# Kernel optimization log

Measured on AMD Instinct MI355X. Metric: run time of the kernel, lower is better.

The kernel has to match this reference:

```python
import jax, jax.numpy as jnp
import numpy as np

IMG_W, IMG_H = 128, 128
N_PTS = 256
MIN_D, MAX_D = 2.0, 6.0
FOCAL = 1.7320508  # 1/tan(fov/2), fov=60deg (FoVPerspectiveCameras default)
SCALING = 0.1      # scaling_factor default
EPS_EA = 1e-10     # pytorch3d EmissionAbsorptionRaymarcher eps


def setup_inputs() -> dict:
    key = jax.random.key(0)
    k1, k2 = jax.random.split(key)
    image3d = jax.random.uniform(k1, (1, 1, 128, 128, 128), jnp.float32)
    opacity = jax.random.uniform(k2, (1, 1, 128, 128, 128), jnp.float32)
    # row-vector camera convention (pytorch3d): p_cam = p_world @ R + T
    R = jnp.zeros((1, 3, 3), jnp.float32).at[:, jnp.arange(3), jnp.arange(3)].set(1.0)
    T = jnp.zeros((1, 3), jnp.float32).at[:, 2].set(4.0)
    return {"image3d": image3d, "opacity": opacity, "R": R, "T": T}


def _trilinear(vol, pts):
    """vol [C,D,H,W]; pts [N,3] xyz in [-1,1] (x->W, y->H, z->D).
    align_corners=True, zero padding outside. Returns [N,C]."""
    C, D, H, W = vol.shape
    x = (pts[:, 0] + 1.0) * 0.5 * (W - 1)
    y = (pts[:, 1] + 1.0) * 0.5 * (H - 1)
    z = (pts[:, 2] + 1.0) * 0.5 * (D - 1)
    x0 = jnp.floor(x); y0 = jnp.floor(y); z0 = jnp.floor(z)
    wx = x - x0; wy = y - y0; wz = z - z0
    vol_flat = vol.reshape(C, -1)
    out = jnp.zeros((pts.shape[0], C), vol.dtype)
    for dz in (0, 1):
        for dy in (0, 1):
            for dx in (0, 1):
                xi = (x0 + dx).astype(jnp.int32)
                yi = (y0 + dy).astype(jnp.int32)
                zi = (z0 + dz).astype(jnp.int32)
                valid = ((xi >= 0) & (xi < W) & (yi >= 0) & (yi < H)
                         & (zi >= 0) & (zi < D))
                w = ((wx if dx else 1.0 - wx) * (wy if dy else 1.0 - wy)
                     * (wz if dz else 1.0 - wz)) * valid.astype(vol.dtype)
                idx = ((jnp.clip(zi, 0, D - 1) * H + jnp.clip(yi, 0, H - 1)) * W
                       + jnp.clip(xi, 0, W - 1))
                vals = jnp.take(vol_flat, idx, axis=1)  # [C,N]
                out = out + w[:, None] * vals.T
    return out


def _forward(image3d, opacity, R, T):
    B = image3d.shape[0]
    features_vol = jnp.repeat(image3d, 3, axis=1)            # [B,3,D,H,W]
    densities_vol = opacity * SCALING                        # [B,1,D,H,W]
    Dv, Hv, Wv = image3d.shape[2:]
    shape = max(image3d.shape[1], image3d.shape[2])
    voxel = 3.0 / shape
    half_extent = voxel * (jnp.array([Wv, Hv, Dv], jnp.float32) - 1.0) / 2.0

    # NDC pixel grid (pytorch3d: +x left, +y up)
    xs = jnp.linspace(1.0, -1.0, IMG_W)
    ys = jnp.linspace(1.0, -1.0, IMG_H)
    gy, gx = jnp.meshgrid(ys, xs, indexing="ij")             # [H,W]
    dirs_cam = jnp.stack([gx / FOCAL, gy / FOCAL, jnp.ones_like(gx)], -1)  # [H,W,3]
    depths = jnp.linspace(MIN_D, MAX_D, N_PTS)               # [P]

    # row-vector transforms: p_world = (p_cam - T) @ R^T
    origins = jnp.einsum("bi,bji->bj", -T, R)                # camera centers [B,3]
    dirs_world = jnp.einsum("hwi,bji->bhwj", dirs_cam, R)    # [B,H,W,3]
    pts = (origins[:, None, None, None, :]
           + depths[None, None, None, :, None] * dirs_world[:, :, :, None, :])
    local = pts / half_extent                                # [B,H,W,P,3]

    pts_flat = local.reshape(B, -1, 3)
    feats = jax.vmap(_trilinear)(features_vol, pts_flat)
    feats = feats.reshape(B, IMG_H, IMG_W, N_PTS, 3)
    dens = jax.vmap(_trilinear)(densities_vol, pts_flat)
    dens = dens.reshape(B, IMG_H, IMG_W, N_PTS)

    # EmissionAbsorption raymarcher
    cum = jnp.cumprod((1.0 + EPS_EA) - dens, axis=-1)
    absorption = jnp.concatenate([jnp.ones_like(cum[..., :1]), cum[..., :-1]], -1)
    weights = dens * absorption
    feat_out = jnp.sum(weights[..., None] * feats, axis=-2)  # [B,H,W,3]
    opac = 1.0 - jnp.prod(1.0 - dens, axis=-1, keepdims=True)
    rgba = jnp.concatenate([feat_out, opac], axis=-1)        # [B,H,W,4]

    screen = jnp.transpose(rgba, (0, 3, 2, 1))               # permute(0,3,2,1)
    gray = screen[:, :3].mean(axis=1, keepdims=True)         # [B,1,W,H]
    st = (gray - gray.mean()) / (gray.std(ddof=1) + 1e-8)    # standardized
    out = (st - st.min() + 1e-8) / (st.max() - st.min() + 1e-8)  # normalized
    return out


def reference(image3d, opacity, R, T):
    return _forward(image3d, opacity, R, T)
```

## Files before the change

### kernel.cpp

```cpp
#include <hip/hip_runtime.h>
#include <math.h>


#define FOCAL 1.7320508f

typedef struct __attribute__((packed, aligned(4))) { float a, b; } f2u;

__global__ __launch_bounds__(1024) void dvr_kernel(
    const float* __restrict__ img, const float* __restrict__ opa,
    const float* __restrict__ Rm, const float* __restrict__ Tv,
    float* __restrict__ g, double* __restrict__ bstats,
    unsigned int* __restrict__ counter, float* __restrict__ out)
{
  const int tid  = threadIdx.x;
  const int lane = tid & 63;
  const int seg  = tid >> 6;
  const int B    = blockIdx.x;
  const int b    = ((B & 7) << 5) | (B >> 3);
  const int h    = b >> 1;
  const int w    = ((b & 1) << 6) | lane;

  const float R00=Rm[0], R01=Rm[1], R02=Rm[2];
  const float R10=Rm[3], R11=Rm[4], R12=Rm[5];
  const float R20=Rm[6], R21=Rm[7], R22=Rm[8];
  const float T0=Tv[0], T1=Tv[1], T2=Tv[2];

  const float ox = -(T0*R00 + T1*R01 + T2*R02);
  const float oy = -(T0*R10 + T1*R11 + T2*R12);
  const float oz = -(T0*R20 + T1*R21 + T2*R22);

  const float gx = 1.0f - (2.0f/127.0f) * (float)w;
  const float gy = 1.0f - (2.0f/127.0f) * (float)h;
  const float dcx = gx * (1.0f/FOCAL);
  const float dcy = gy * (1.0f/FOCAL);
  const float dwx = dcx*R00 + dcy*R01 + R02;
  const float dwy = dcx*R10 + dcy*R11 + R12;
  const float dwz = dcx*R20 + dcy*R21 + R22;

  const float s_he = (1.0f/1.48828125f) * 63.5f;
  const float ax = dwx * s_he, bxc = ox * s_he + 63.5f;
  const float ay = dwy * s_he, byc = oy * s_he + 63.5f;
  const float az = dwz * s_he, bzc = oz * s_he + 63.5f;

  const int p0 = seg << 4;

  float lp = 1.0f;
  float accl = 0.0f;

  #pragma unroll 4
  for (int j = 0; j < 16; ++j) {
    const float depth = 2.0f + (4.0f/255.0f) * (float)(p0 + j);
    const float x = bxc + depth * ax;
    const float y = byc + depth * ay;
    const float z = bzc + depth * az;
    const float x0f = floorf(x), y0f = floorf(y), z0f = floorf(z);
    const float wx = x - x0f, wy = y - y0f, wz = z - z0f;
    const int x0 = (int)x0f, y0 = (int)y0f, z0 = (int)z0f;

    float feat = 0.0f, dens = 0.0f;
    if (x0 >= -1 && x0 <= 127 && y0 >= -1 && y0 <= 127 &&
        z0 >= -1 && z0 <= 127) {
      const float fx0 = (x0 >= 0)   ? (1.0f - wx) : 0.0f;
      const float fx1 = (x0 <= 126) ? wx          : 0.0f;
      const float fy0 = (y0 >= 0)   ? (1.0f - wy) : 0.0f;
      const float fy1 = (y0 <= 126) ? wy          : 0.0f;
      const float fz0 = (z0 >= 0)   ? (1.0f - wz) : 0.0f;
      const float fz1 = (z0 <= 126) ? wz          : 0.0f;
      const int iy0 = ((y0 >= 0)   ? y0     : 0)   << 7;
      const int iy1 = ((y0 <= 126) ? y0 + 1 : 127) << 7;
      const int iz0 = ((z0 >= 0)   ? z0     : 0)   << 14;
      const int iz1 = ((z0 <= 126) ? z0 + 1 : 127) << 14;
      const int ixp = (x0 >= 0) ? ((x0 <= 126) ? x0 : 126) : 0;

      const int b00 = iz0 + iy0 + ixp, b01 = iz0 + iy1 + ixp;
      const int b10 = iz1 + iy0 + ixp, b11 = iz1 + iy1 + ixp;
      const float w00 = fz0*fy0, w01 = fz0*fy1, w10 = fz1*fy0, w11 = fz1*fy1;

      const f2u q00 = *(const f2u*)(img + b00);
      const f2u q01 = *(const f2u*)(img + b01);
      const f2u q10 = *(const f2u*)(img + b10);
      const f2u q11 = *(const f2u*)(img + b11);
      const f2u r00 = *(const f2u*)(opa + b00);
      const f2u r01 = *(const f2u*)(opa + b01);
      const f2u r10 = *(const f2u*)(opa + b10);
      const f2u r11 = *(const f2u*)(opa + b11);

      const bool cA = (x0 < 127);
      const bool cB = (x0 >= 0);

      feat = w00*(fx0*(cA ? q00.a : q00.b) + fx1*(cB ? q00.b : q00.a))
           + w01*(fx0*(cA ? q01.a : q01.b) + fx1*(cB ? q01.b : q01.a))
           + w10*(fx0*(cA ? q10.a : q10.b) + fx1*(cB ? q10.b : q10.a))
           + w11*(fx0*(cA ? q11.a : q11.b) + fx1*(cB ? q11.b : q11.a));
      dens = w00*(fx0*(cA ? r00.a : r00.b) + fx1*(cB ? r00.b : r00.a))
           + w01*(fx0*(cA ? r01.a : r01.b) + fx1*(cB ? r01.b : r01.a))
           + w10*(fx0*(cA ? r10.a : r10.b) + fx1*(cB ? r10.b : r10.a))
           + w11*(fx0*(cA ? r11.a : r11.b) + fx1*(cB ? r11.b : r11.a));
    }
    const float d = dens * 0.1f;
    accl += feat * d * lp;
    lp   *= (1.0f - d);
  }

  __shared__ float2 slp[16][64];
  slp[seg][lane] = make_float2(accl, lp);
  __syncthreads();

  if (tid < 64) {
    float T = 1.0f, acc = 0.0f;
    #pragma unroll
    for (int s = 0; s < 16; ++s) {
      const float2 v = slp[s][tid];
      acc += v.x * T;
      T *= v.y;
    }
    const int ww = ((b & 1) << 6) | tid;
    g[(ww << 7) + h] = acc;

    double sum = (double)acc;
    double sq  = (double)acc * (double)acc;
    float mn = acc, mx = acc;
    #pragma unroll
    for (int off = 32; off >= 1; off >>= 1) {
      sum += __shfl_xor(sum, off, 64);
      sq  += __shfl_xor(sq,  off, 64);
      mn = fminf(mn, __shfl_xor(mn, off, 64));
      mx = fmaxf(mx, __shfl_xor(mx, off, 64));
    }
    if (tid == 0) {
      bstats[(b << 2) + 0] = sum;
      bstats[(b << 2) + 1] = sq;
      bstats[(b << 2) + 2] = (double)mn;
      bstats[(b << 2) + 3] = (double)mx;
    }
  }
  __syncthreads();

  __shared__ int is_last;
  if (tid == 0) {
    __threadfence();
    const unsigned int old = atomicAdd(counter, 1u);
    const unsigned int base = old - 255u;
    is_last = (base == 0xAAAAAAAAu || base == 0u) ? 1 : 0;
  }
  __syncthreads();
  if (!is_last) return;
  __threadfence();

  double S = 0.0, Q = 0.0;
  float MN = 3.402823466e38f, MX = -3.402823466e38f;
  if (tid < 256) {
    S  = bstats[(tid << 2) + 0];
    Q  = bstats[(tid << 2) + 1];
    MN = (float)bstats[(tid << 2) + 2];
    MX = (float)bstats[(tid << 2) + 3];
  }
  #pragma unroll
  for (int off = 32; off >= 1; off >>= 1) {
    S += __shfl_xor(S, off, 64);
    Q += __shfl_xor(Q, off, 64);
    MN = fminf(MN, __shfl_xor(MN, off, 64));
    MX = fmaxf(MX, __shfl_xor(MX, off, 64));
  }
  __shared__ double rs[16], rq[16];
  __shared__ float rmn[16], rmx[16];
  if (lane == 0) { rs[seg] = S; rq[seg] = Q; rmn[seg] = MN; rmx[seg] = MX; }
  __syncthreads();

  __shared__ float cs[3];
  if (tid == 0) {
    double St = 0.0, Qt = 0.0;
    float MNt = rmn[0], MXt = rmx[0];
    #pragma unroll
    for (int i = 0; i < 4; ++i) {
      St += rs[i]; Qt += rq[i];
      MNt = fminf(MNt, rmn[i]); MXt = fmaxf(MXt, rmx[i]);
    }
    const double mean = St / 16384.0;
    double var = (Qt - 16384.0 * mean * mean) / 16383.0;
    if (var < 0.0) var = 0.0;
    const float sdev = (float)sqrt(var) + 1e-8f;
    cs[0] = MNt;
    cs[1] = 1.0f / sdev;
    cs[2] = 1.0f / ((MXt - MNt) / sdev + 1e-8f);
  }
  __syncthreads();

  const float mnv = cs[0], invs = cs[1], sc = cs[2];
  for (int i = tid; i < 16384; i += 1024) {
    out[i] = ((g[i] - mnv) * invs + 1e-8f) * sc;
  }
}

extern "C" void kernel_launch(void* const* d_in, const int* in_sizes, int n_in,
                              void* d_out, int out_size, void* d_ws, size_t ws_size,
                              hipStream_t stream) {
  const float* img = (const float*)d_in[0];
  const float* opa = (const float*)d_in[1];
  const float* Rm  = (const float*)d_in[2];
  const float* Tv  = (const float*)d_in[3];
  float* out = (float*)d_out;

  char* wsb = (char*)d_ws;
  float*        g       = (float*)wsb;
  double*       bstats  = (double*)(wsb + 65536);
  unsigned int* counter = (unsigned int*)(wsb + 65536 + 8192);

  dvr_kernel<<<256, 1024, 0, stream>>>(img, opa, Rm, Tv, g, bstats, counter, out);
}
```

Before: 94.33 us.

## Pack image and opacity into interleaved fp16 volume before raymarching

```diff
diff --git a/kernel.cpp b/kernel.cpp
--- a/kernel.cpp
+++ b/kernel.cpp
@@ -1,13 +1,38 @@
 #include <hip/hip_runtime.h>
+#include <hip/hip_fp16.h>
 #include <math.h>
 
 
 #define FOCAL 1.7320508f
 
-typedef struct __attribute__((packed, aligned(4))) { float a, b; } f2u;
+typedef struct __attribute__((packed, aligned(4))) { unsigned int lo, hi; } u2u;
+
+static __device__ __forceinline__ float2 h2f(unsigned int u) {
+  __half2 h = *reinterpret_cast<__half2*>(&u);
+  return __half22float2(h);
+}
+
+__global__ __launch_bounds__(256) void pack_kernel(
+    const float4* __restrict__ img, const float4* __restrict__ opa,
+    uint4* __restrict__ dst)
+{
+  const int i = blockIdx.x * 256 + threadIdx.x;
+  const float4 f = img[i];
+  const float4 o = opa[i];
+  const __half2 h0 = __floats2half2_rn(f.x, o.x);
+  const __half2 h1 = __floats2half2_rn(f.y, o.y);
+  const __half2 h2 = __floats2half2_rn(f.z, o.z);
+  const __half2 h3 = __floats2half2_rn(f.w, o.w);
+  uint4 r;
+  r.x = *(const unsigned int*)&h0;
+  r.y = *(const unsigned int*)&h1;
+  r.z = *(const unsigned int*)&h2;
+  r.w = *(const unsigned int*)&h3;
+  dst[i] = r;
+}
 
 __global__ __launch_bounds__(1024) void dvr_kernel(
-    const float* __restrict__ img, const float* __restrict__ opa,
+    const unsigned int* __restrict__ vol,
     const float* __restrict__ Rm, const float* __restrict__ Tv,
     float* __restrict__ g, double* __restrict__ bstats,
     unsigned int* __restrict__ counter, float* __restrict__ out)
@@ -76,26 +101,32 @@
       const int b10 = iz1 + iy0 + ixp, b11 = iz1 + iy1 + ixp;
       const float w00 = fz0*fy0, w01 = fz0*fy1, w10 = fz1*fy0, w11 = fz1*fy1;
 
-      const f2u q00 = *(const f2u*)(img + b00);
-      const f2u q01 = *(const f2u*)(img + b01);
-      const f2u q10 = *(const f2u*)(img + b10);
-      const f2u q11 = *(const f2u*)(img + b11);
-      const f2u r00 = *(const f2u*)(opa + b00);
-      const f2u r01 = *(const f2u*)(opa + b01);
-      const f2u r10 = *(const f2u*)(opa + b10);
-      const f2u r11 = *(const f2u*)(opa + b11);
+      const u2u q00 = *(const u2u*)(vol + b00);
+      const u2u q01 = *(const u2u*)(vol + b01);
+      const u2u q10 = *(const u2u*)(vol + b10);
+      const u2u q11 = *(const u2u*)(vol + b11);
 
       const bool cA = (x0 < 127);
       const bool cB = (x0 >= 0);
 
-      feat = w00*(fx0*(cA ? q00.a : q00.b) + fx1*(cB ? q00.b : q00.a))
-           + w01*(fx0*(cA ? q01.a : q01.b) + fx1*(cB ? q01.b : q01.a))
-           + w10*(fx0*(cA ? q10.a : q10.b) + fx1*(cB ? q10.b : q10.a))
-           + w11*(fx0*(cA ? q11.a : q11.b) + fx1*(cB ? q11.b : q11.a));
-      dens = w00*(fx0*(cA ? r00.a : r00.b) + fx1*(cB ? r00.b : r00.a))
-           + w01*(fx0*(cA ? r01.a : r01.b) + fx1*(cB ? r01.b : r01.a))
-           + w10*(fx0*(cA ? r10.a : r10.b) + fx1*(cB ? r10.b : r10.a))
-           + w11*(fx0*(cA ? r11.a : r11.b) + fx1*(cB ? r11.b : r11.a));
+      const unsigned int a00 = cA ? q00.lo : q00.hi, b00s = cB ? q00.hi : q00.lo;
+      const unsigned int a01 = cA ? q01.lo : q01.hi, b01s = cB ? q01.hi : q01.lo;
+      const unsigned int a10 = cA ? q10.lo : q10.hi, b10s = cB ? q10.hi : q10.lo;
+      const unsigned int a11 = cA ? q11.lo : q11.hi, b11s = cB ? q11.hi : q11.lo;
+
+      const float2 fa00 = h2f(a00), fb00 = h2f(b00s);
+      const float2 fa01 = h2f(a01), fb01 = h2f(b01s);
+      const float2 fa10 = h2f(a10), fb10 = h2f(b10s);
+      const float2 fa11 = h2f(a11), fb11 = h2f(b11s);
+
+      feat = w00*(fx0*fa00.x + fx1*fb00.x)
+           + w01*(fx0*fa01.x + fx1*fb01.x)
+           + w10*(fx0*fa10.x + fx1*fb10.x)
+           + w11*(fx0*fa11.x + fx1*fb11.x);
+      dens = w00*(fx0*fa00.y + fx1*fb00.y)
+           + w01*(fx0*fa01.y + fx1*fb01.y)
+           + w10*(fx0*fa10.y + fx1*fb10.y)
+           + w11*(fx0*fa11.y + fx1*fb11.y);
     }
     const float d = dens * 0.1f;
     accl += feat * d * lp;
@@ -205,6 +236,9 @@
   float*        g       = (float*)wsb;
   double*       bstats  = (double*)(wsb + 65536);
   unsigned int* counter = (unsigned int*)(wsb + 65536 + 8192);
-
-  dvr_kernel<<<256, 1024, 0, stream>>>(img, opa, Rm, Tv, g, bstats, counter, out);
-}
+  unsigned int* vol     = (unsigned int*)(wsb + (1 << 20));
+
+  pack_kernel<<<2048, 256, 0, stream>>>((const float4*)img, (const float4*)opa,
+                                        (uint4*)vol);
+  dvr_kernel<<<256, 1024, 0, stream>>>(vol, Rm, Tv, g, bstats, counter, out);
+}
```

Result: slower. 98.75 us (+4.7%).

## Stage per-chunk volume bricks in shared memory as packed half2

Applied to the files above, without the earlier changes.

```diff
diff --git a/kernel.cpp b/kernel.cpp
--- a/kernel.cpp
+++ b/kernel.cpp
@@ -1,10 +1,19 @@
 #include <hip/hip_runtime.h>
+#include <hip/hip_fp16.h>
 #include <math.h>
 
 
 #define FOCAL 1.7320508f
 
-typedef struct __attribute__((packed, aligned(4))) { float a, b; } f2u;
+#define BZ 12
+#define BYW 4
+#define BW 176
+#define ROWSTRIDE (BYW*BW)
+
+static __device__ __forceinline__ float2 h2f(unsigned int u) {
+  __half2 h = *reinterpret_cast<__half2*>(&u);
+  return __half22float2(h);
+}
 
 __global__ __launch_bounds__(1024) void dvr_kernel(
     const float* __restrict__ img, const float* __restrict__ opa,
@@ -14,7 +23,7 @@
 {
   const int tid  = threadIdx.x;
   const int lane = tid & 63;
-  const int seg  = tid >> 6;
+  const int sub  = tid >> 6;
   const int B    = blockIdx.x;
   const int b    = ((B & 7) << 5) | (B >> 3);
   const int h    = b >> 1;
@@ -42,14 +51,64 @@
   const float ay = dwy * s_he, byc = oy * s_he + 63.5f;
   const float az = dwz * s_he, bzc = oz * s_he + 63.5f;
 
-  const int p0 = seg << 4;
-
-  float lp = 1.0f;
-  float accl = 0.0f;
-
-  #pragma unroll 4
-  for (int j = 0; j < 16; ++j) {
-    const float depth = 2.0f + (4.0f/255.0f) * (float)(p0 + j);
+  __shared__ unsigned int brick[BZ*ROWSTRIDE];
+  __shared__ float2 slp[16][64];
+
+  float rayAcc = 0.0f, rayT = 1.0f;
+
+  const float dstep = 4.0f/255.0f;
+
+  #pragma unroll 1
+  for (int c = 0; c < 16; ++c) {
+    const float dA = 2.0f + dstep * (float)(c << 4);
+    const float dB = 2.0f + dstep * (float)((c << 4) + 15);
+    const float xAe = bxc + dA*ax, xBe = bxc + dB*ax;
+    const float yAe = byc + dA*ay, yBe = byc + dB*ay;
+    const float zAe = bzc + dA*az, zBe = bzc + dB*az;
+
+    float xmn = fminf(xAe, xBe), xmx = fmaxf(xAe, xBe);
+    float ymnA = yAe, ymnB = yBe;
+    float zmn = fminf(zAe, zBe), zmx = fmaxf(zAe, zBe);
+    #pragma unroll
+    for (int off = 32; off >= 1; off >>= 1) {
+      xmn  = fminf(xmn,  __shfl_xor(xmn,  off, 64));
+      xmx  = fmaxf(xmx,  __shfl_xor(xmx,  off, 64));
+      ymnA = fminf(ymnA, __shfl_xor(ymnA, off, 64));
+      ymnB = fminf(ymnB, __shfl_xor(ymnB, off, 64));
+      zmn  = fminf(zmn,  __shfl_xor(zmn,  off, 64));
+      zmx  = fmaxf(zmx,  __shfl_xor(zmx,  off, 64));
+    }
+    const int x_lo = (int)floorf(xmn);
+    const int z_lo = (int)floorf(zmn);
+    int zcnt = (int)floorf(zmx) + 2 - z_lo;
+    zcnt = (zcnt < 1) ? 1 : ((zcnt > BZ) ? BZ : zcnt);
+
+    const float zg = zBe - zAe;
+    const float invzg = (fabsf(zg) > 1e-6f) ? (1.0f / zg) : 0.0f;
+    const float ySlope = (ymnB - ymnA) * invzg;
+
+    const bool live = (zmx >= -1.0f) && (zmn <= 128.0f) &&
+                      (xmx >= -1.0f) && (xmn <= 128.0f);
+
+    if (live) {
+      const int n = zcnt * ROWSTRIDE;
+      for (int idx = tid; idx < n; idx += 1024) {
+        const int dz = idx / ROWSTRIDE;
+        const int r2 = idx - dz * ROWSTRIDE;
+        const int dy = r2 / BW;
+        const int dx = r2 - dy * BW;
+        const int ylos = (int)floorf(ymnA + ((float)(z_lo + dz) + 0.5f - zAe) * ySlope) - 1;
+        int gz_ = z_lo + dz;  gz_ = (gz_ < 0) ? 0 : ((gz_ > 127) ? 127 : gz_);
+        int gy_ = ylos + dy;  gy_ = (gy_ < 0) ? 0 : ((gy_ > 127) ? 127 : gy_);
+        int gx_ = x_lo + dx;  gx_ = (gx_ < 0) ? 0 : ((gx_ > 127) ? 127 : gx_);
+        const int a = (((gz_ << 7) + gy_) << 7) + gx_;
+        const __half2 hp = __floats2half2_rn(img[a], opa[a]);
+        brick[idx] = *(const unsigned int*)&hp;
+      }
+    }
+    __syncthreads();
+
+    const float depth = 2.0f + dstep * (float)((c << 4) + sub);
     const float x = bxc + depth * ax;
     const float y = byc + depth * ay;
     const float z = bzc + depth * az;
@@ -66,54 +125,57 @@
       const float fy1 = (y0 <= 126) ? wy          : 0.0f;
       const float fz0 = (z0 >= 0)   ? (1.0f - wz) : 0.0f;
       const float fz1 = (z0 <= 126) ? wz          : 0.0f;
-      const int iy0 = ((y0 >= 0)   ? y0     : 0)   << 7;
-      const int iy1 = ((y0 <= 126) ? y0 + 1 : 127) << 7;
-      const int iz0 = ((z0 >= 0)   ? z0     : 0)   << 14;
-      const int iz1 = ((z0 <= 126) ? z0 + 1 : 127) << 14;
-      const int ixp = (x0 >= 0) ? ((x0 <= 126) ? x0 : 126) : 0;
-
-      const int b00 = iz0 + iy0 + ixp, b01 = iz0 + iy1 + ixp;
-      const int b10 = iz1 + iy0 + ixp, b11 = iz1 + iy1 + ixp;
+
+      int bx = x0 - x_lo;  bx = (bx < 0) ? 0 : ((bx > BW-2) ? (BW-2) : bx);
+      int bz0 = z0 - z_lo; bz0 = (bz0 < 0) ? 0 : ((bz0 > zcnt-1) ? (zcnt-1) : bz0);
+      int bz1 = bz0 + 1;   bz1 = (bz1 > zcnt-1) ? (zcnt-1) : bz1;
+
+      const int ylo0 = (int)floorf(ymnA + ((float)(z_lo + bz0) + 0.5f - zAe) * ySlope) - 1;
+      const int ylo1 = (int)floorf(ymnA + ((float)(z_lo + bz1) + 0.5f - zAe) * ySlope) - 1;
+      int dy00 = y0     - ylo0; dy00 = (dy00 < 0) ? 0 : ((dy00 > 3) ? 3 : dy00);
+      int dy01 = y0 + 1 - ylo0; dy01 = (dy01 < 0) ? 0 : ((dy01 > 3) ? 3 : dy01);
+      int dy10 = y0     - ylo1; dy10 = (dy10 < 0) ? 0 : ((dy10 > 3) ? 3 : dy10);
+      int dy11 = y0 + 1 - ylo1; dy11 = (dy11 < 0) ? 0 : ((dy11 > 3) ? 3 : dy11);
+
+      const int e00 = (bz0*BYW + dy00)*BW + bx;
+      const int e01 = (bz0*BYW + dy01)*BW + bx;
+      const int e10 = (bz1*BYW + dy10)*BW + bx;
+      const int e11 = (bz1*BYW + dy11)*BW + bx;
+
+      const float2 v00a = h2f(brick[e00]), v00b = h2f(brick[e00+1]);
+      const float2 v01a = h2f(brick[e01]), v01b = h2f(brick[e01+1]);
+      const float2 v10a = h2f(brick[e10]), v10b = h2f(brick[e10+1]);
+      const float2 v11a = h2f(brick[e11]), v11b = h2f(brick[e11+1]);
+
       const float w00 = fz0*fy0, w01 = fz0*fy1, w10 = fz1*fy0, w11 = fz1*fy1;
-
-      const f2u q00 = *(const f2u*)(img + b00);
-      const f2u q01 = *(const f2u*)(img + b01);
-      const f2u q10 = *(const f2u*)(img + b10);
-      const f2u q11 = *(const f2u*)(img + b11);
-      const f2u r00 = *(const f2u*)(opa + b00);
-      const f2u r01 = *(const f2u*)(opa + b01);
-      const f2u r10 = *(const f2u*)(opa + b10);
-      const f2u r11 = *(const f2u*)(opa + b11);
-
-      const bool cA = (x0 < 127);
-      const bool cB = (x0 >= 0);
-
-      feat = w00*(fx0*(cA ? q00.a : q00.b) + fx1*(cB ? q00.b : q00.a))
-           + w01*(fx0*(cA ? q01.a : q01.b) + fx1*(cB ? q01.b : q01.a))
-           + w10*(fx0*(cA ? q10.a : q10.b) + fx1*(cB ? q10.b : q10.a))
-           + w11*(fx0*(cA ? q11.a : q11.b) + fx1*(cB ? q11.b : q11.a));
-      dens = w00*(fx0*(cA ? r00.a : r00.b) + fx1*(cB ? r00.b : r00.a))
-           + w01*(fx0*(cA ? r01.a : r01.b) + fx1*(cB ? r01.b : r01.a))
-           + w10*(fx0*(cA ? r10.a : r10.b) + fx1*(cB ? r10.b : r10.a))
-           + w11*(fx0*(cA ? r11.a : r11.b) + fx1*(cB ? r11.b : r11.a));
+      feat = w00*(fx0*v00a.x + fx1*v00b.x)
+           + w01*(fx0*v01a.x + fx1*v01b.x)
+           + w10*(fx0*v10a.x + fx1*v10b.x)
+           + w11*(fx0*v11a.x + fx1*v11b.x);
+      dens = w00*(fx0*v00a.y + fx1*v00b.y)
+           + w01*(fx0*v01a.y + fx1*v01b.y)
+           + w10*(fx0*v10a.y + fx1*v10b.y)
+           + w11*(fx0*v11a.y + fx1*v11b.y);
     }
     const float d = dens * 0.1f;
-    accl += feat * d * lp;
-    lp   *= (1.0f - d);
-  }
-
-  __shared__ float2 slp[16][64];
-  slp[seg][lane] = make_float2(accl, lp);
-  __syncthreads();
+    slp[sub][lane] = make_float2(feat * d, 1.0f - d);
+    __syncthreads();
+
+    if (tid < 64) {
+      float a_ = 0.0f, T_ = 1.0f;
+      #pragma unroll
+      for (int s = 0; s < 16; ++s) {
+        const float2 v = slp[s][tid];
+        a_ += v.x * T_;
+        T_ *= v.y;
+      }
+      rayAcc += rayT * a_;
+      rayT   *= T_;
+    }
+  }
 
   if (tid < 64) {
-    float T = 1.0f, acc = 0.0f;
-    #pragma unroll
-    for (int s = 0; s < 16; ++s) {
-      const float2 v = slp[s][tid];
-      acc += v.x * T;
-      T *= v.y;
-    }
+    const float acc = rayAcc;
     const int ww = ((b & 1) << 6) | tid;
     g[(ww << 7) + h] = acc;
 
@@ -164,7 +226,7 @@
   }
   __shared__ double rs[16], rq[16];
   __shared__ float rmn[16], rmx[16];
-  if (lane == 0) { rs[seg] = S; rq[seg] = Q; rmn[seg] = MN; rmx[seg] = MX; }
+  if (lane == 0) { rs[sub] = S; rq[sub] = Q; rmn[sub] = MN; rmx[sub] = MX; }
   __syncthreads();
 
   __shared__ float cs[3];
```

Result: slower. 149.4 us (+58.4%).

## Precompute per-sample y/z trilinear terms once per wavefront and broadcast via readlane

Applied to the files above, without the earlier changes.

```diff
diff --git a/kernel.cpp b/kernel.cpp
--- a/kernel.cpp
+++ b/kernel.cpp
@@ -43,63 +43,133 @@
   const float az = dwz * s_he, bzc = oz * s_he + 63.5f;
 
   const int p0 = seg << 4;
+  const float dstep = 4.0f/255.0f;
 
   float lp = 1.0f;
   float accl = 0.0f;
 
-  #pragma unroll 4
-  for (int j = 0; j < 16; ++j) {
-    const float depth = 2.0f + (4.0f/255.0f) * (float)(p0 + j);
-    const float x = bxc + depth * ax;
-    const float y = byc + depth * ay;
-    const float z = bzc + depth * az;
-    const float x0f = floorf(x), y0f = floorf(y), z0f = floorf(z);
-    const float wx = x - x0f, wy = y - y0f, wz = z - z0f;
-    const int x0 = (int)x0f, y0 = (int)y0f, z0 = (int)z0f;
-
-    float feat = 0.0f, dens = 0.0f;
-    if (x0 >= -1 && x0 <= 127 && y0 >= -1 && y0 <= 127 &&
-        z0 >= -1 && z0 <= 127) {
-      const float fx0 = (x0 >= 0)   ? (1.0f - wx) : 0.0f;
-      const float fx1 = (x0 <= 126) ? wx          : 0.0f;
-      const float fy0 = (y0 >= 0)   ? (1.0f - wy) : 0.0f;
-      const float fy1 = (y0 <= 126) ? wy          : 0.0f;
-      const float fz0 = (z0 >= 0)   ? (1.0f - wz) : 0.0f;
-      const float fz1 = (z0 <= 126) ? wz          : 0.0f;
-      const int iy0 = ((y0 >= 0)   ? y0     : 0)   << 7;
-      const int iy1 = ((y0 <= 126) ? y0 + 1 : 127) << 7;
-      const int iz0 = ((z0 >= 0)   ? z0     : 0)   << 14;
-      const int iz1 = ((z0 <= 126) ? z0 + 1 : 127) << 14;
-      const int ixp = (x0 >= 0) ? ((x0 <= 126) ? x0 : 126) : 0;
-
-      const int b00 = iz0 + iy0 + ixp, b01 = iz0 + iy1 + ixp;
-      const int b10 = iz1 + iy0 + ixp, b11 = iz1 + iy1 + ixp;
-      const float w00 = fz0*fy0, w01 = fz0*fy1, w10 = fz1*fy0, w11 = fz1*fy1;
-
-      const f2u q00 = *(const f2u*)(img + b00);
-      const f2u q01 = *(const f2u*)(img + b01);
-      const f2u q10 = *(const f2u*)(img + b10);
-      const f2u q11 = *(const f2u*)(img + b11);
-      const f2u r00 = *(const f2u*)(opa + b00);
-      const f2u r01 = *(const f2u*)(opa + b01);
-      const f2u r10 = *(const f2u*)(opa + b10);
-      const f2u r11 = *(const f2u*)(opa + b11);
-
+  if (R10 == 0.0f && R20 == 0.0f) {
+    const int jp = lane & 15;
+    const float dp = 2.0f + dstep * (float)(p0 + jp);
+    const float yp = byc + dp * ay;
+    const float zp = bzc + dp * az;
+    const float y0f = floorf(yp), z0f = floorf(zp);
+    const float wyp = yp - y0f, wzp = zp - z0f;
+    const int y0 = (int)y0f, z0 = (int)z0f;
+    const float fy0 = (y0 >=  0 && y0 <= 127) ? (1.0f - wyp) : 0.0f;
+    const float fy1 = (y0 >= -1 && y0 <= 126) ? wyp          : 0.0f;
+    const float fz0 = (z0 >=  0 && z0 <= 127) ? (1.0f - wzp) : 0.0f;
+    const float fz1 = (z0 >= -1 && z0 <= 126) ? wzp          : 0.0f;
+    const int y1t = y0 + 1, z1t = z0 + 1;
+    const int iy0 = ((y0  < 0) ? 0 : ((y0  > 127) ? 127 : y0 )) << 7;
+    const int iy1 = ((y1t < 0) ? 0 : ((y1t > 127) ? 127 : y1t)) << 7;
+    const int iz0 = ((z0  < 0) ? 0 : ((z0  > 127) ? 127 : z0 )) << 14;
+    const int iz1 = ((z1t < 0) ? 0 : ((z1t > 127) ? 127 : z1t)) << 14;
+    const float w00v = fz0*fy0, w01v = fz0*fy1, w10v = fz1*fy0, w11v = fz1*fy1;
+    const int rb00v = iz0 + iy0, rb01v = iz0 + iy1;
+    const int rb10v = iz1 + iy0, rb11v = iz1 + iy1;
+
+    #pragma unroll
+    for (int j = 0; j < 16; ++j) {
+      const float w00 = __int_as_float(__builtin_amdgcn_readlane(__float_as_int(w00v), j));
+      const float w01 = __int_as_float(__builtin_amdgcn_readlane(__float_as_int(w01v), j));
+      const float w10 = __int_as_float(__builtin_amdgcn_readlane(__float_as_int(w10v), j));
+      const float w11 = __int_as_float(__builtin_amdgcn_readlane(__float_as_int(w11v), j));
+      const int rb00 = __builtin_amdgcn_readlane(rb00v, j);
+      const int rb01 = __builtin_amdgcn_readlane(rb01v, j);
+      const int rb10 = __builtin_amdgcn_readlane(rb10v, j);
+      const int rb11 = __builtin_amdgcn_readlane(rb11v, j);
+
+      const float depth = 2.0f + dstep * (float)(p0 + j);
+      const float x = bxc + depth * ax;
+      const float x0f = floorf(x);
+      const float wx = x - x0f;
+      const int x0 = (int)x0f;
+      const float fx0 = (x0 >=  0 && x0 <= 127) ? (1.0f - wx) : 0.0f;
+      const float fx1 = (x0 >= -1 && x0 <= 126) ? wx          : 0.0f;
       const bool cA = (x0 < 127);
       const bool cB = (x0 >= 0);
-
-      feat = w00*(fx0*(cA ? q00.a : q00.b) + fx1*(cB ? q00.b : q00.a))
-           + w01*(fx0*(cA ? q01.a : q01.b) + fx1*(cB ? q01.b : q01.a))
-           + w10*(fx0*(cA ? q10.a : q10.b) + fx1*(cB ? q10.b : q10.a))
-           + w11*(fx0*(cA ? q11.a : q11.b) + fx1*(cB ? q11.b : q11.a));
-      dens = w00*(fx0*(cA ? r00.a : r00.b) + fx1*(cB ? r00.b : r00.a))
-           + w01*(fx0*(cA ? r01.a : r01.b) + fx1*(cB ? r01.b : r01.a))
-           + w10*(fx0*(cA ? r10.a : r10.b) + fx1*(cB ? r10.b : r10.a))
-           + w11*(fx0*(cA ? r11.a : r11.b) + fx1*(cB ? r11.b : r11.a));
-    }
-    const float d = dens * 0.1f;
-    accl += feat * d * lp;
-    lp   *= (1.0f - d);
+      const float wa = cB ? (cA ? fx0 : fx1) : fx1;
+      const float wb = cB ? (cA ? fx1 : fx0) : fx0;
+      const int ixp = (x0 < 0) ? 0 : ((x0 > 126) ? 126 : x0);
+
+      const f2u q00 = *(const f2u*)(img + rb00 + ixp);
+      const f2u q01 = *(const f2u*)(img + rb01 + ixp);
+      const f2u q10 = *(const f2u*)(img + rb10 + ixp);
+      const f2u q11 = *(const f2u*)(img + rb11 + ixp);
+      const f2u r00 = *(const f2u*)(opa + rb00 + ixp);
+      const f2u r01 = *(const f2u*)(opa + rb01 + ixp);
+      const f2u r10 = *(const f2u*)(opa + rb10 + ixp);
+      const f2u r11 = *(const f2u*)(opa + rb11 + ixp);
+
+      const float feat = w00*(wa*q00.a + wb*q00.b)
+                       + w01*(wa*q01.a + wb*q01.b)
+                       + w10*(wa*q10.a + wb*q10.b)
+                       + w11*(wa*q11.a + wb*q11.b);
+      const float dens = w00*(wa*r00.a + wb*r00.b)
+                       + w01*(wa*r01.a + wb*r01.b)
+                       + w10*(wa*r10.a + wb*r10.b)
+                       + w11*(wa*r11.a + wb*r11.b);
+
+      const float d = dens * 0.1f;
+      accl += feat * d * lp;
+      lp   *= (1.0f - d);
+    }
+  } else {
+    #pragma unroll 4
+    for (int j = 0; j < 16; ++j) {
+      const float depth = 2.0f + dstep * (float)(p0 + j);
+      const float x = bxc + depth * ax;
+      const float y = byc + depth * ay;
+      const float z = bzc + depth * az;
+      const float x0f = floorf(x), y0f = floorf(y), z0f = floorf(z);
+      const float wx = x - x0f, wy = y - y0f, wz = z - z0f;
+      const int x0 = (int)x0f, y0 = (int)y0f, z0 = (int)z0f;
+
+      float feat = 0.0f, dens = 0.0f;
+      if (x0 >= -1 && x0 <= 127 && y0 >= -1 && y0 <= 127 &&
+          z0 >= -1 && z0 <= 127) {
+        const float fx0 = (x0 >= 0)   ? (1.0f - wx) : 0.0f;
+        const float fx1 = (x0 <= 126) ? wx          : 0.0f;
+        const float fy0 = (y0 >= 0)   ? (1.0f - wy) : 0.0f;
+        const float fy1 = (y0 <= 126) ? wy          : 0.0f;
+        const float fz0 = (z0 >= 0)   ? (1.0f - wz) : 0.0f;
+        const float fz1 = (z0 <= 126) ? wz          : 0.0f;
+        const int iy0 = ((y0 >= 0)   ? y0     : 0)   << 7;
+        const int iy1 = ((y0 <= 126) ? y0 + 1 : 127) << 7;
+        const int iz0 = ((z0 >= 0)   ? z0     : 0)   << 14;
+        const int iz1 = ((z0 <= 126) ? z0 + 1 : 127) << 14;
+        const int ixp = (x0 >= 0) ? ((x0 <= 126) ? x0 : 126) : 0;
+
+        const int b00 = iz0 + iy0 + ixp, b01 = iz0 + iy1 + ixp;
+        const int b10 = iz1 + iy0 + ixp, b11 = iz1 + iy1 + ixp;
+        const float w00 = fz0*fy0, w01 = fz0*fy1, w10 = fz1*fy0, w11 = fz1*fy1;
+
+        const f2u q00 = *(const f2u*)(img + b00);
+        const f2u q01 = *(const f2u*)(img + b01);
+        const f2u q10 = *(const f2u*)(img + b10);
+        const f2u q11 = *(const f2u*)(img + b11);
+        const f2u r00 = *(const f2u*)(opa + b00);
+        const f2u r01 = *(const f2u*)(opa + b01);
+        const f2u r10 = *(const f2u*)(opa + b10);
+        const f2u r11 = *(const f2u*)(opa + b11);
+
+        const bool cA = (x0 < 127);
+        const bool cB = (x0 >= 0);
+
+        feat = w00*(fx0*(cA ? q00.a : q00.b) + fx1*(cB ? q00.b : q00.a))
+             + w01*(fx0*(cA ? q01.a : q01.b) + fx1*(cB ? q01.b : q01.a))
+             + w10*(fx0*(cA ? q10.a : q10.b) + fx1*(cB ? q10.b : q10.a))
+             + w11*(fx0*(cA ? q11.a : q11.b) + fx1*(cB ? q11.b : q11.a));
+        dens = w00*(fx0*(cA ? r00.a : r00.b) + fx1*(cB ? r00.b : r00.a))
+             + w01*(fx0*(cA ? r01.a : r01.b) + fx1*(cB ? r01.b : r01.a))
+             + w10*(fx0*(cA ? r10.a : r10.b) + fx1*(cB ? r10.b : r10.a))
+             + w11*(fx0*(cA ? r11.a : r11.b) + fx1*(cB ? r11.b : r11.a));
+      }
+      const float d = dens * 0.1f;
+      accl += feat * d * lp;
+      lp   *= (1.0f - d);
+    }
   }
 
   __shared__ float2 slp[16][64];
```

Measured after the change: 97.50 us. +3.4%, slower.
